# Kernel optimization log

Hardware: AMD Instinct MI355X
Metric: run time of the kernel (lower is better)

## Reference

```python
import jax, jax.numpy as jnp
import numpy as np

N_NODES = 200000
N_EDGES = 6400000
N_GRAPHS = 1000


def setup_inputs() -> dict:
    key = jax.random.key(0)
    ks = jax.random.split(key, 8)
    x = jax.random.normal(ks[0], (N_NODES, 2), dtype=jnp.float32)
    edge_index = jax.random.randint(ks[1], (2, N_EDGES), 0, N_NODES, dtype=jnp.int32)
    batch = jnp.sort(jax.random.randint(ks[2], (N_NODES,), 0, N_GRAPHS, dtype=jnp.int32))
    W1 = jax.random.normal(ks[3], (2, 16), dtype=jnp.float32) * (1.0 / np.sqrt(2))
    b1 = jnp.zeros((16,), jnp.float32)
    W2 = jax.random.normal(ks[4], (16, 32), dtype=jnp.float32) * (1.0 / np.sqrt(16))
    b2 = jnp.zeros((32,), jnp.float32)
    Wfc1 = jax.random.normal(ks[5], (32, 16), dtype=jnp.float32) * (1.0 / np.sqrt(32))
    bfc1 = jnp.zeros((16,), jnp.float32)
    Wfc2 = jax.random.normal(ks[6], (16, 1), dtype=jnp.float32) * (1.0 / np.sqrt(16))
    bfc2 = jnp.zeros((1,), jnp.float32)
    return {"x": x, "edge_index": edge_index, "batch": batch,
            "W1": W1, "b1": b1, "W2": W2, "b2": b2,
            "Wfc1": Wfc1, "bfc1": bfc1, "Wfc2": Wfc2, "bfc2": bfc2}


def _gcn_norm(edge_index, n_nodes):
    # PyG GCNConv default: add self loops, symmetric normalization.
    loops = jnp.arange(n_nodes, dtype=edge_index.dtype)
    src = jnp.concatenate([edge_index[0], loops])  # message source (row)
    dst = jnp.concatenate([edge_index[1], loops])  # aggregation target (col)
    deg = jax.ops.segment_sum(jnp.ones_like(dst, jnp.float32), dst, num_segments=n_nodes)
    dinv = jnp.where(deg > 0, jax.lax.rsqrt(jnp.maximum(deg, 1.0)), 0.0)
    norm = dinv[src] * dinv[dst]  # [E + N]
    return src, dst, norm


def _gcn_conv(h, W, b, src, dst, norm, n_nodes):
    h = h @ W                                      # transform first (small width)
    msg = h[src] * norm[:, None]                   # gather + scale: [E+N, F]
    out = jax.ops.segment_sum(msg, dst, num_segments=n_nodes)
    return out + b


def reference(x, edge_index, batch, W1, b1, W2, b2, Wfc1, bfc1, Wfc2, bfc2):
    n = x.shape[0]
    src, dst, norm = _gcn_norm(edge_index, n)
    h = jax.nn.relu(_gcn_conv(x, W1, b1, src, dst, norm, n))
    h = jax.nn.relu(_gcn_conv(h, W2, b2, src, dst, norm, n))
    # global_mean_pool over graph ids
    sums = jax.ops.segment_sum(h, batch, num_segments=N_GRAPHS)
    cnts = jax.ops.segment_sum(jnp.ones((n,), h.dtype), batch, num_segments=N_GRAPHS)
    pooled = sums / jnp.maximum(cnts, 1.0)[:, None]  # [G, 32]
    out = jax.nn.relu(pooled @ Wfc1 + bfc1)
    out = out @ Wfc2 + bfc2                          # [G, 1]
    return out.squeeze(-1)
```

## Files before the change

kernel.cpp:

```cpp
#include <hip/hip_runtime.h>
#include <hip/hip_fp16.h>

static inline size_t align256(size_t x) { return (x + 255) & ~size_t(255); }

#define CAP 36864

__global__ __launch_bounds__(1024) void k_scatter(const int* __restrict__ ei,
                                                  int* __restrict__ bcursor,
                                                  unsigned* __restrict__ bdata, int E) {
    __shared__ int lcount[256];
    __shared__ int gbase[256];
    int t = threadIdx.x;
    if (t < 256) lcount[t] = 0;
    __syncthreads();
    int chunk = blockIdx.x * 16384;
    int srcv[16], bkt[16], rank[16], dl[16];
#pragma unroll
    for (int k = 0; k < 8; ++k) {
        int e = chunk + k * 2048 + 2 * t;
        int k2 = 2 * k;
        bkt[k2] = -1; bkt[k2 + 1] = -1;
        if (e < E) {
            int2 sp = *(const int2*)(ei + e);
            int2 dp = *(const int2*)(ei + E + e);
            srcv[k2] = sp.x; bkt[k2] = dp.x >> 10; dl[k2] = dp.x & 1023;
            rank[k2] = atomicAdd(&lcount[bkt[k2]], 1);
            srcv[k2 + 1] = sp.y; bkt[k2 + 1] = dp.y >> 10; dl[k2 + 1] = dp.y & 1023;
            rank[k2 + 1] = atomicAdd(&lcount[bkt[k2 + 1]], 1);
        }
    }
    __syncthreads();
    if (t < 256) {
        int c = lcount[t];
        gbase[t] = t * CAP + (c ? atomicAdd(&bcursor[t], c) : 0);
    }
    __syncthreads();
#pragma unroll
    for (int k = 0; k < 16; ++k) {
        if (bkt[k] >= 0)
            bdata[gbase[bkt[k]] + rank[k]] = ((unsigned)dl[k] << 18) | (unsigned)srcv[k];
    }
}

__global__ __launch_bounds__(1024) void k_build1(const unsigned* __restrict__ bdata,
                                                 const int* __restrict__ bcursor,
                                                 int* __restrict__ row_ptr,
                                                 float* __restrict__ dinv,
                                                 const float* __restrict__ x,
                                                 float2* __restrict__ xt,
                                                 int N, int E, int NBv) {
    __shared__ int hist[1024];
    __shared__ int sums[256];
    __shared__ int bsc[256];
    int bkt = blockIdx.x;
    int t = threadIdx.x;
    if (t < 256) bsc[t] = (t < NBv) ? bcursor[t] : 0;
    __syncthreads();
    for (int off = 1; off < 256; off <<= 1) {
        int xv = 0;
        if (t < 256 && t >= off) xv = bsc[t - off];
        __syncthreads();
        if (t < 256) bsc[t] += xv;
        __syncthreads();
    }
    int count = bcursor[bkt];
    int tb = bsc[bkt] - count;
    int fs = bkt * CAP;
    int node0 = bkt << 10;
    int nn = N - node0; if (nn > 1024) nn = 1024;
    hist[t] = 0;
    __syncthreads();
    for (int e = t; e < count; e += 1024)
        atomicAdd(&hist[bdata[fs + e] >> 18], 1);
    __syncthreads();
    int v0 = 0, v1 = 0, v2 = 0, v3 = 0, s = 0;
    if (t < 256) {
        int b4 = t * 4;
        v0 = hist[b4]; v1 = hist[b4 + 1]; v2 = hist[b4 + 2]; v3 = hist[b4 + 3];
        s = v0 + v1 + v2 + v3;
        sums[t] = s;
    }
    __syncthreads();
    for (int off = 1; off < 256; off <<= 1) {
        int xv = 0;
        if (t < 256 && t >= off) xv = sums[t - off];
        __syncthreads();
        if (t < 256) sums[t] += xv;
        __syncthreads();
    }
    if (t < 256) {
        int b4 = t * 4;
        int e0 = sums[t] - s;
        int e1 = e0 + v0, e2 = e1 + v1, e3 = e2 + v2;
        if (b4 < nn)     { row_ptr[node0 + b4]     = tb + e0; dinv[node0 + b4]     = rsqrtf((float)v0 + 1.f); }
        if (b4 + 1 < nn) { row_ptr[node0 + b4 + 1] = tb + e1; dinv[node0 + b4 + 1] = rsqrtf((float)v1 + 1.f); }
        if (b4 + 2 < nn) { row_ptr[node0 + b4 + 2] = tb + e2; dinv[node0 + b4 + 2] = rsqrtf((float)v2 + 1.f); }
        if (b4 + 3 < nn) { row_ptr[node0 + b4 + 3] = tb + e3; dinv[node0 + b4 + 3] = rsqrtf((float)v3 + 1.f); }
    }
    if (bkt == NBv - 1 && t == 0) row_ptr[N] = E;
    __syncthreads();
    for (int i = t; i < nn; i += 1024) {
        int node = node0 + i;
        float d2 = rsqrtf((float)hist[i] + 1.f);
        xt[node] = make_float2(x[node * 2] * d2, x[node * 2 + 1] * d2);
    }
}

__global__ __launch_bounds__(1024) void k_build2(const unsigned* __restrict__ bdata,
                                                 const int* __restrict__ bcursor,
                                                 const int* __restrict__ row_ptr,
                                                 const float2* __restrict__ xt,
                                                 const float* __restrict__ W1,
                                                 const float* __restrict__ b1,
                                                 int* __restrict__ col,
                                                 uint4* __restrict__ ht,
                                                 int N, int E, int NBv) {
    __shared__ int curs[1024];
    __shared__ int cstart[1024];
    __shared__ int stage[CAP];
    __shared__ float w1s[32];
    __shared__ float b1s[16];
    int bkt = blockIdx.x;
    int t = threadIdx.x;
    if (t < 32) w1s[t] = W1[t];
    if (t < 16) b1s[t] = b1[t];
    int count = bcursor[bkt];
    int fs = bkt * CAP;
    int node0 = bkt << 10;
    int nn = N - node0; if (nn > 1024) nn = 1024;
    int tb = row_ptr[node0];
    int sl0 = (t < nn) ? (row_ptr[node0 + t] - tb) : 0;
    curs[t] = sl0;
    cstart[t] = sl0;
    __syncthreads();
    for (int e = t; e < count; e += 1024) {
        unsigned p = bdata[fs + e];
        int dl = p >> 18;
        int pos = atomicAdd(&curs[dl], 1);
        stage[pos] = (int)(p & 0x3FFFFu);
    }
    __syncthreads();
    for (int i = t; i < count; i += 1024)
        col[tb + i] = stage[i];
    if (t < nn) {
        int node = node0 + t;
        int sl = cstart[t], el = curs[t];
        float a0 = 0.f, a1 = 0.f;
        int e = sl;
        for (; e + 8 <= el; e += 8) {
            int c[8];
#pragma unroll
            for (int k = 0; k < 8; ++k) c[k] = stage[e + k];
            float2 v[8];
#pragma unroll
            for (int k = 0; k < 8; ++k) v[k] = xt[c[k]];
#pragma unroll
            for (int k = 0; k < 8; ++k) { a0 += v[k].x; a1 += v[k].y; }
        }
        for (; e < el; ++e) {
            float2 v = xt[stage[e]];
            a0 += v.x; a1 += v.y;
        }
        float2 sf = xt[node];
        a0 += sf.x; a1 += sf.y;
        float dv = rsqrtf((float)(el - sl) + 1.f);
        a0 *= dv; a1 *= dv;
        __half2 hv[8];
#pragma unroll
        for (int f2 = 0; f2 < 8; ++f2) {
            float v0 = fmaxf(a0 * w1s[2 * f2]     + a1 * w1s[16 + 2 * f2]     + b1s[2 * f2],     0.f) * dv;
            float v1 = fmaxf(a0 * w1s[2 * f2 + 1] + a1 * w1s[16 + 2 * f2 + 1] + b1s[2 * f2 + 1], 0.f) * dv;
            hv[f2] = __floats2half2_rn(v0, v1);
        }
        ht[(size_t)node * 2]     = *reinterpret_cast<uint4*>(&hv[0]);
        ht[(size_t)node * 2 + 1] = *reinterpret_cast<uint4*>(&hv[4]);
    }
}

__global__ __launch_bounds__(256) void k_gather2(const int* __restrict__ rp,
                                                 const int* __restrict__ col,
                                                 const __half2* __restrict__ ht,
                                                 const float* __restrict__ dinv,
                                                 float* __restrict__ agg, int N) {
    int gt = blockIdx.x * 256 + threadIdx.x;
    int node = gt >> 3;
    int fq = gt & 7;
    if (node >= N) return;
    int rs = rp[node], re = rp[node + 1];
    const __half2* __restrict__ base = ht + fq;
    float ax = 0.f, ay = 0.f;
    int e = rs;
    for (; e + 16 <= re; e += 16) {
        int c[16];
#pragma unroll
        for (int k = 0; k < 16; ++k) c[k] = __builtin_nontemporal_load(col + e + k);
        float2 v[16];
#pragma unroll
        for (int k = 0; k < 16; ++k) v[k] = __half22float2(base[(size_t)c[k] * 8]);
#pragma unroll
        for (int k = 0; k < 16; ++k) { ax += v[k].x; ay += v[k].y; }
    }
    for (; e + 8 <= re; e += 8) {
        int c[8];
#pragma unroll
        for (int k = 0; k < 8; ++k) c[k] = __builtin_nontemporal_load(col + e + k);
        float2 v[8];
#pragma unroll
        for (int k = 0; k < 8; ++k) v[k] = __half22float2(base[(size_t)c[k] * 8]);
#pragma unroll
        for (int k = 0; k < 8; ++k) { ax += v[k].x; ay += v[k].y; }
    }
    for (; e < re; ++e) {
        float2 v = __half22float2(base[(size_t)col[e] * 8]);
        ax += v.x; ay += v.y;
    }
    {
        float2 v = __half22float2(base[(size_t)node * 8]);
        ax += v.x; ay += v.y;
    }
    float dv = dinv[node];
    __builtin_nontemporal_store(ax * dv, agg + (size_t)node * 16 + 2 * fq);
    __builtin_nontemporal_store(ay * dv, agg + (size_t)node * 16 + 2 * fq + 1);
}

__global__ __launch_bounds__(256) void k_trans_pool(const float* __restrict__ agg,
                                                    const float* __restrict__ W2,
                                                    const float* __restrict__ b2,
                                                    const int* __restrict__ batch,
                                                    float* __restrict__ gsum, int N) {
    __shared__ float aggs[64][17];
    __shared__ float h2s[64][33];
    __shared__ float w2s[512];
    __shared__ float b2s[32];
    __shared__ int   bids[64];
    int t = threadIdx.x;
    if (t < 128) ((float4*)w2s)[t] = ((const float4*)W2)[t];
    if (t < 32)  b2s[t] = b2[t];
    int node0 = blockIdx.x * 64;
    if (t < 64)  bids[t] = (node0 + t < N) ? batch[node0 + t] : -1;
    {
        int nl = t >> 2, q = t & 3;
        int node = node0 + nl;
        float4 v = make_float4(0.f, 0.f, 0.f, 0.f);
        if (node < N) v = *(const float4*)(agg + (size_t)node * 16 + (size_t)q * 4);
        int c0 = q * 4;
        aggs[nl][c0] = v.x; aggs[nl][c0 + 1] = v.y;
        aggs[nl][c0 + 2] = v.z; aggs[nl][c0 + 3] = v.w;
    }
    __syncthreads();
    {
        int nl = t >> 2;
        int jq = (t & 3) * 8;
        float o[8];
#pragma unroll
        for (int j = 0; j < 8; ++j) o[j] = b2s[jq + j];
#pragma unroll
        for (int k = 0; k < 16; ++k) {
            float a = aggs[nl][k];
#pragma unroll
            for (int j = 0; j < 8; ++j) o[j] += a * w2s[k * 32 + jq + j];
        }
#pragma unroll
        for (int j = 0; j < 8; ++j) h2s[nl][jq + j] = fmaxf(o[j], 0.f);
    }
    __syncthreads();
    if (t < 128) {
        int j = t & 31, seg = t >> 5;
        int nbeg = seg * 16, nend = nbeg + 16;
        float acc = 0.f;
        int cur = bids[nbeg];
        for (int n2 = nbeg; n2 < nend; ++n2) {
            int b = bids[n2];
            if (b != cur) {
                if (cur >= 0) atomicAdd(&gsum[(size_t)cur * 32 + j], acc);
                acc = 0.f; cur = b;
            }
            if (b >= 0) acc += h2s[n2][j];
        }
        if (cur >= 0) atomicAdd(&gsum[(size_t)cur * 32 + j], acc);
    }
}

__global__ void k_final(const float* __restrict__ gsum, const int* __restrict__ batch,
                        const float* __restrict__ Wfc1, const float* __restrict__ bfc1,
                        const float* __restrict__ Wfc2, const float* __restrict__ bfc2,
                        float* __restrict__ out, int G, int N) {
    int g = blockIdx.x * blockDim.x + threadIdx.x;
    if (g >= G) return;
    int lo = 0, hi = N;
    while (lo < hi) { int m = (lo + hi) >> 1; if (batch[m] < g) lo = m + 1; else hi = m; }
    int s = lo;
    lo = s; hi = N;
    while (lo < hi) { int m = (lo + hi) >> 1; if (batch[m] < g + 1) lo = m + 1; else hi = m; }
    float cnt = (float)(lo - s);
    float inv = 1.f / fmaxf(cnt, 1.f);
    float p[32];
#pragma unroll
    for (int i = 0; i < 32; ++i) p[i] = gsum[(size_t)g * 32 + i] * inv;
    float o = bfc2[0];
#pragma unroll
    for (int j = 0; j < 16; ++j) {
        float a = bfc1[j];
#pragma unroll
        for (int i = 0; i < 32; ++i) a += p[i] * Wfc1[i * 16 + j];
        o += fmaxf(a, 0.f) * Wfc2[j];
    }
    out[g] = o;
}

extern "C" void kernel_launch(void* const* d_in, const int* in_sizes, int n_in,
                              void* d_out, int out_size, void* d_ws, size_t ws_size,
                              hipStream_t stream) {
    const float* x     = (const float*)d_in[0];
    const int*   ei    = (const int*)d_in[1];
    const int*   batch = (const int*)d_in[2];
    const float* W1    = (const float*)d_in[3];
    const float* b1    = (const float*)d_in[4];
    const float* W2    = (const float*)d_in[5];
    const float* b2    = (const float*)d_in[6];
    const float* Wfc1  = (const float*)d_in[7];
    const float* bfc1  = (const float*)d_in[8];
    const float* Wfc2  = (const float*)d_in[9];
    const float* bfc2  = (const float*)d_in[10];
    float* out = (float*)d_out;

    const int N = in_sizes[0] / 2;
    const int E = in_sizes[1] / 2;
    const int G = out_size;
    const int NBv = (N + 1023) >> 10;

    char* ws = (char*)d_ws;
    size_t off = 0;
    float* dinv    = (float*)(ws + off); off += align256((size_t)N * 4);
    int*   row_ptr = (int*)(ws + off);   off += align256((size_t)(N + 1) * 4);
    int*   bcursor = (int*)(ws + off);   size_t z0 = off; off += align256(256 * 4);
    float* gsum    = (float*)(ws + off); off += align256((size_t)G * 32 * 4);
    size_t zlen = off - z0;
    float2* xt     = (float2*)(ws + off); off += align256((size_t)N * 8);
    __half2* ht    = (__half2*)(ws + off); off += align256((size_t)N * 32);
    float* agg     = (float*)(ws + off); off += align256((size_t)N * 16 * 4);
    int*   col     = (int*)(ws + off);   off += align256((size_t)E * 4);
    unsigned* bdata = (unsigned*)(ws + off); off += align256((size_t)NBv * CAP * 4);

    const int BS = 256;

    hipMemsetAsync(bcursor, 0, zlen, stream);

    k_scatter<<<(E + 16383) / 16384, 1024, 0, stream>>>(ei, bcursor, bdata, E);
    k_build1<<<NBv, 1024, 0, stream>>>(bdata, bcursor, row_ptr, dinv, x, xt, N, E, NBv);
    k_build2<<<NBv, 1024, 0, stream>>>(bdata, bcursor, row_ptr, xt, W1, b1, col,
                                       (uint4*)ht, N, E, NBv);

    k_gather2<<<((size_t)N * 8 + 255) / 256, 256, 0, stream>>>(row_ptr, col, (const __half2*)ht,
                                                               dinv, agg, N);
    k_trans_pool<<<(N + 63) / 64, 256, 0, stream>>>(agg, W2, b2, batch, gsum, N);

    k_final<<<(G + BS - 1) / BS, BS, 0, stream>>>(gsum, batch, Wfc1, bfc1, Wfc2, bfc2,
                                                  out, G, N);
}
```

Before: 227.9 us.

## Fuse layer-2 gather with W2 transform and graph pooling; drop dinv buffer

Merges the second-layer neighbor gather, the 16x32 W2 transform (done through wave shuffles across the 8 lanes that hold a node's features) and the mean-pool atomics into one kernel. This removes the round trip of the N x 16 float agg buffer and one kernel launch. dinv is now recomputed from row_ptr differences instead of being stored and reloaded. When a whole wave belongs to one graph, partial sums are reduced with shuffles before the atomics. Otherwise it falls back to per-lane atomics, which may add atomic contention compared with the earlier segmented per-block reduction.

```diff
diff --git a/kernel.cpp b/kernel.cpp
--- a/kernel.cpp
+++ b/kernel.cpp
@@ -45,7 +45,6 @@
 __global__ __launch_bounds__(1024) void k_build1(const unsigned* __restrict__ bdata,
                                                  const int* __restrict__ bcursor,
                                                  int* __restrict__ row_ptr,
-                                                 float* __restrict__ dinv,
                                                  const float* __restrict__ x,
                                                  float2* __restrict__ xt,
                                                  int N, int E, int NBv) {
@@ -92,10 +91,10 @@
         int b4 = t * 4;
         int e0 = sums[t] - s;
         int e1 = e0 + v0, e2 = e1 + v1, e3 = e2 + v2;
-        if (b4 < nn)     { row_ptr[node0 + b4]     = tb + e0; dinv[node0 + b4]     = rsqrtf((float)v0 + 1.f); }
-        if (b4 + 1 < nn) { row_ptr[node0 + b4 + 1] = tb + e1; dinv[node0 + b4 + 1] = rsqrtf((float)v1 + 1.f); }
-        if (b4 + 2 < nn) { row_ptr[node0 + b4 + 2] = tb + e2; dinv[node0 + b4 + 2] = rsqrtf((float)v2 + 1.f); }
-        if (b4 + 3 < nn) { row_ptr[node0 + b4 + 3] = tb + e3; dinv[node0 + b4 + 3] = rsqrtf((float)v3 + 1.f); }
+        if (b4 < nn)     row_ptr[node0 + b4]     = tb + e0;
+        if (b4 + 1 < nn) row_ptr[node0 + b4 + 1] = tb + e1;
+        if (b4 + 2 < nn) row_ptr[node0 + b4 + 2] = tb + e2;
+        if (b4 + 3 < nn) row_ptr[node0 + b4 + 3] = tb + e3;
     }
     if (bkt == NBv - 1 && t == 0) row_ptr[N] = E;
     __syncthreads();
@@ -177,16 +176,25 @@
     }
 }
 
-__global__ __launch_bounds__(256) void k_gather2(const int* __restrict__ rp,
-                                                 const int* __restrict__ col,
-                                                 const __half2* __restrict__ ht,
-                                                 const float* __restrict__ dinv,
-                                                 float* __restrict__ agg, int N) {
-    int gt = blockIdx.x * 256 + threadIdx.x;
+__global__ __launch_bounds__(256) void k_gather2_fused(const int* __restrict__ rp,
+                                                       const int* __restrict__ col,
+                                                       const __half2* __restrict__ ht,
+                                                       const int* __restrict__ batch,
+                                                       const float* __restrict__ W2,
+                                                       const float* __restrict__ b2,
+                                                       float* __restrict__ gsum, int N) {
+    __shared__ float w2s[512];
+    __shared__ float b2s[32];
+    int t = threadIdx.x;
+    if (t < 128) ((float4*)w2s)[t] = ((const float4*)W2)[t];
+    if (t < 32)  b2s[t] = b2[t];
+    __syncthreads();
+    int gt = blockIdx.x * 256 + t;
     int node = gt >> 3;
     int fq = gt & 7;
-    if (node >= N) return;
-    int rs = rp[node], re = rp[node + 1];
+    bool valid = node < N;
+    int rs = 0, re = 0;
+    if (valid) { rs = rp[node]; re = rp[node + 1]; }
     const __half2* __restrict__ base = ht + fq;
     float ax = 0.f, ay = 0.f;
     int e = rs;
@@ -214,70 +222,52 @@
         float2 v = __half22float2(base[(size_t)col[e] * 8]);
         ax += v.x; ay += v.y;
     }
-    {
+    if (valid) {
         float2 v = __half22float2(base[(size_t)node * 8]);
         ax += v.x; ay += v.y;
     }
-    float dv = dinv[node];
-    __builtin_nontemporal_store(ax * dv, agg + (size_t)node * 16 + 2 * fq);
-    __builtin_nontemporal_store(ay * dv, agg + (size_t)node * 16 + 2 * fq + 1);
-}
-
-__global__ __launch_bounds__(256) void k_trans_pool(const float* __restrict__ agg,
-                                                    const float* __restrict__ W2,
-                                                    const float* __restrict__ b2,
-                                                    const int* __restrict__ batch,
-                                                    float* __restrict__ gsum, int N) {
-    __shared__ float aggs[64][17];
-    __shared__ float h2s[64][33];
-    __shared__ float w2s[512];
-    __shared__ float b2s[32];
-    __shared__ int   bids[64];
-    int t = threadIdx.x;
-    if (t < 128) ((float4*)w2s)[t] = ((const float4*)W2)[t];
-    if (t < 32)  b2s[t] = b2[t];
-    int node0 = blockIdx.x * 64;
-    if (t < 64)  bids[t] = (node0 + t < N) ? batch[node0 + t] : -1;
-    {
-        int nl = t >> 2, q = t & 3;
-        int node = node0 + nl;
-        float4 v = make_float4(0.f, 0.f, 0.f, 0.f);
-        if (node < N) v = *(const float4*)(agg + (size_t)node * 16 + (size_t)q * 4);
-        int c0 = q * 4;
-        aggs[nl][c0] = v.x; aggs[nl][c0 + 1] = v.y;
-        aggs[nl][c0 + 2] = v.z; aggs[nl][c0 + 3] = v.w;
-    }
-    __syncthreads();
-    {
-        int nl = t >> 2;
-        int jq = (t & 3) * 8;
-        float o[8];
-#pragma unroll
-        for (int j = 0; j < 8; ++j) o[j] = b2s[jq + j];
-#pragma unroll
-        for (int k = 0; k < 16; ++k) {
-            float a = aggs[nl][k];
-#pragma unroll
-            for (int j = 0; j < 8; ++j) o[j] += a * w2s[k * 32 + jq + j];
-        }
-#pragma unroll
-        for (int j = 0; j < 8; ++j) h2s[nl][jq + j] = fmaxf(o[j], 0.f);
-    }
-    __syncthreads();
-    if (t < 128) {
-        int j = t & 31, seg = t >> 5;
-        int nbeg = seg * 16, nend = nbeg + 16;
-        float acc = 0.f;
-        int cur = bids[nbeg];
-        for (int n2 = nbeg; n2 < nend; ++n2) {
-            int b = bids[n2];
-            if (b != cur) {
-                if (cur >= 0) atomicAdd(&gsum[(size_t)cur * 32 + j], acc);
-                acc = 0.f; cur = b;
-            }
-            if (b >= 0) acc += h2s[n2][j];
-        }
-        if (cur >= 0) atomicAdd(&gsum[(size_t)cur * 32 + j], acc);
+    float dv = valid ? rsqrtf((float)(re - rs) + 1.f) : 0.f;
+    float a0 = ax * dv, a1 = ay * dv;
+
+    int wl = t & 63;
+    int ob = wl & 56;
+    int jq = fq * 4;
+    float o0 = b2s[jq], o1 = b2s[jq + 1], o2 = b2s[jq + 2], o3 = b2s[jq + 3];
+#pragma unroll
+    for (int k = 0; k < 8; ++k) {
+        float ae = __shfl(a0, ob + k);
+        float ao = __shfl(a1, ob + k);
+        const float* we = w2s + (2 * k) * 32 + jq;
+        const float* wo = w2s + (2 * k + 1) * 32 + jq;
+        o0 += ae * we[0] + ao * wo[0];
+        o1 += ae * we[1] + ao * wo[1];
+        o2 += ae * we[2] + ao * wo[2];
+        o3 += ae * we[3] + ao * wo[3];
+    }
+    o0 = fmaxf(o0, 0.f); o1 = fmaxf(o1, 0.f); o2 = fmaxf(o2, 0.f); o3 = fmaxf(o3, 0.f);
+    if (!valid) { o0 = o1 = o2 = o3 = 0.f; }
+
+    int b = valid ? batch[node] : -1;
+    int bfirst = __shfl(b, 0);
+    unsigned long long uni = __ballot(b == bfirst);
+    if (uni == ~0ull) {
+        o0 += __shfl_xor(o0, 8); o0 += __shfl_xor(o0, 16); o0 += __shfl_xor(o0, 32);
+        o1 += __shfl_xor(o1, 8); o1 += __shfl_xor(o1, 16); o1 += __shfl_xor(o1, 32);
+        o2 += __shfl_xor(o2, 8); o2 += __shfl_xor(o2, 16); o2 += __shfl_xor(o2, 32);
+        o3 += __shfl_xor(o3, 8); o3 += __shfl_xor(o3, 16); o3 += __shfl_xor(o3, 32);
+        if (wl < 8 && bfirst >= 0) {
+            float* g = gsum + (size_t)bfirst * 32 + jq;
+            atomicAdd(g,     o0);
+            atomicAdd(g + 1, o1);
+            atomicAdd(g + 2, o2);
+            atomicAdd(g + 3, o3);
+        }
+    } else if (b >= 0) {
+        float* g = gsum + (size_t)b * 32 + jq;
+        atomicAdd(g,     o0);
+        atomicAdd(g + 1, o1);
+        atomicAdd(g + 2, o2);
+        atomicAdd(g + 3, o3);
     }
 }
 
@@ -331,14 +321,12 @@
 
     char* ws = (char*)d_ws;
     size_t off = 0;
-    float* dinv    = (float*)(ws + off); off += align256((size_t)N * 4);
     int*   row_ptr = (int*)(ws + off);   off += align256((size_t)(N + 1) * 4);
     int*   bcursor = (int*)(ws + off);   size_t z0 = off; off += align256(256 * 4);
     float* gsum    = (float*)(ws + off); off += align256((size_t)G * 32 * 4);
     size_t zlen = off - z0;
     float2* xt     = (float2*)(ws + off); off += align256((size_t)N * 8);
     __half2* ht    = (__half2*)(ws + off); off += align256((size_t)N * 32);
-    float* agg     = (float*)(ws + off); off += align256((size_t)N * 16 * 4);
     int*   col     = (int*)(ws + off);   off += align256((size_t)E * 4);
     unsigned* bdata = (unsigned*)(ws + off); off += align256((size_t)NBv * CAP * 4);
 
@@ -347,13 +335,13 @@
     hipMemsetAsync(bcursor, 0, zlen, stream);
 
     k_scatter<<<(E + 16383) / 16384, 1024, 0, stream>>>(ei, bcursor, bdata, E);
-    k_build1<<<NBv, 1024, 0, stream>>>(bdata, bcursor, row_ptr, dinv, x, xt, N, E, NBv);
+    k_build1<<<NBv, 1024, 0, stream>>>(bdata, bcursor, row_ptr, x, xt, N, E, NBv);
     k_build2<<<NBv, 1024, 0, stream>>>(bdata, bcursor, row_ptr, xt, W1, b1, col,
                                        (uint4*)ht, N, E, NBv);
 
-    k_gather2<<<((size_t)N * 8 + 255) / 256, 256, 0, stream>>>(row_ptr, col, (const __half2*)ht,
-                                                               dinv, agg, N);
-    k_trans_pool<<<(N + 63) / 64, 256, 0, stream>>>(agg, W2, b2, batch, gsum, N);
+    k_gather2_fused<<<((size_t)N * 8 + 255) / 256, 256, 0, stream>>>(row_ptr, col,
+                                                                     (const __half2*)ht,
+                                                                     batch, W2, b2, gsum, N);
 
     k_final<<<(G + BS - 1) / BS, BS, 0, stream>>>(gsum, batch, Wfc1, bfc1, Wfc2, bfc2,
                                                   out, G, N);
```

New measurement: 218.8 us. -4.0%, faster.
